# Kernel optimization log

Measured on AMD Instinct MI355X. Metric: run time of the kernel, lower is better.

## Reference

```python
import jax, jax.numpy as jnp
import numpy as np

N = 6144
IN_FEATS = 512
OUT_FEATS = 64
NHEADS = 8
ALPHA = 0.2
NEG_BIG = -9e15


def setup_inputs() -> dict:
    key = jax.random.key(0)
    k_x, k_adj, k_w, k_a1, k_a2 = jax.random.split(key, 5)
    x = jax.random.normal(k_x, (N, IN_FEATS), dtype=jnp.float32)
    adj = jax.random.randint(k_adj, (N, N), 0, 2, dtype=jnp.int32)
    # xavier_uniform with gain=1.414 ~ sqrt(2)
    gain = 1.414
    bw = gain * np.sqrt(6.0 / (IN_FEATS + OUT_FEATS))
    W = jax.random.uniform(k_w, (NHEADS, IN_FEATS, OUT_FEATS), jnp.float32, -bw, bw)
    ba = gain * np.sqrt(6.0 / (OUT_FEATS + 1))
    a1 = jax.random.uniform(k_a1, (NHEADS, OUT_FEATS), jnp.float32, -ba, ba)
    a2 = jax.random.uniform(k_a2, (NHEADS, OUT_FEATS), jnp.float32, -ba, ba)
    return {"x": x, "adj": adj, "W": W, "a1": a1, "a2": a2}


def reference(x, adj, W, a1, a2):
    # h: [H, N, F] per-head projected features
    h = jnp.einsum("ni,hif->hnf", x, W)
    s1 = jnp.einsum("hnf,hf->hn", h, a1)  # [H, N]
    s2 = jnp.einsum("hnf,hf->hn", h, a2)  # [H, N]
    # outer-sum score [H, N, N], leaky-relu, adjacency mask, row softmax
    scores = jax.nn.leaky_relu(s1[:, :, None] + s2[:, None, :], negative_slope=ALPHA)
    scores = jnp.where(adj[None] > 0, scores, NEG_BIG)
    att = jax.nn.softmax(scores, axis=-1)
    out = jnp.einsum("hnm,hmf->hnf", att, h)  # [H, N, F]
    # concat heads: [N, H*F]
    out = jnp.transpose(out, (1, 0, 2)).reshape(N, NHEADS * OUT_FEATS)
    return jax.nn.elu(out)
```

## Files before the change

kernel.cpp:

```cpp
#include <hip/hip_runtime.h>
#include <hip/hip_bf16.h>
#include <stdint.h>

#define N_NODES 6144
#define IN_F    512
#define OUT_F   64
#define NH      8
#define ALPHA   0.2f
#define L2E     1.4426950408889634f
#define NTILES  (N_NODES / 64)

typedef __attribute__((ext_vector_type(8))) short bf16x8;
typedef __attribute__((ext_vector_type(8))) _Float16 f16x8;
typedef __attribute__((ext_vector_type(4))) float f32x4;

#define MFMA16B(a, b, c) __builtin_amdgcn_mfma_f32_16x16x32_bf16(a, b, c, 0, 0, 0)
#define MFMA16H(a, b, c) __builtin_amdgcn_mfma_f32_16x16x32_f16(a, b, c, 0, 0, 0)

__device__ __forceinline__ unsigned short f2bf(float f) {
    uint32_t u = __float_as_uint(f);
    u += 0x7fffu + ((u >> 16) & 1u);
    return (unsigned short)(u >> 16);
}
__device__ __forceinline__ float bf2f(unsigned short h) {
    return __uint_as_float(((uint32_t)h) << 16);
}
__device__ __forceinline__ unsigned short f16b(float f) {
    union { _Float16 h; unsigned short u; } c;
    c.h = (_Float16)f;
    return c.u;
}
__device__ __forceinline__ uint32_t encf(float x) {
    int i = __float_as_int(x);
    return (i >= 0) ? ((uint32_t)i | 0x80000000u) : ~(uint32_t)i;
}
__device__ __forceinline__ float decf(uint32_t u) {
    int i = (u & 0x80000000u) ? (int)(u & 0x7FFFFFFFu) : ~(int)u;
    return __int_as_float(i);
}

__global__ __launch_bounds__(256) void k_prep(
    const float* __restrict__ x, unsigned short* __restrict__ xh,
    unsigned short* __restrict__ xl,
    const float* __restrict__ W, unsigned short* __restrict__ wthF,
    unsigned short* __restrict__ wtlF, uint32_t* __restrict__ s2mu,
    const int* __restrict__ adj, unsigned long long* __restrict__ bmT)
{
    const int bid = blockIdx.x;
    if (bid < 2048) {
        const int stride = 2048 * 256;
        for (int idx = bid * 256 + threadIdx.x; idx < N_NODES * N_NODES;
             idx += stride) {
            unsigned long long b = __ballot(adj[idx] > 0);
            if ((threadIdx.x & 63) == 0) {
                int r = idx / N_NODES;
                int cb = (idx % N_NODES) >> 6;
                bmT[(size_t)cb * N_NODES + r] = b;
            }
        }
    } else if (bid < 5120) {
        int i = (bid - 2048) * 256 + threadIdx.x;
        float4 v = ((const float4*)x)[i];
        float vv[4] = {v.x, v.y, v.z, v.w};
        unsigned short h4[4], l4[4];
#pragma unroll
        for (int c = 0; c < 4; ++c) {
            unsigned short hb = f2bf(vv[c]);
            h4[c] = hb;
            l4[c] = f2bf(vv[c] - bf2f(hb));
        }
        ((ushort4*)xh)[i] = make_ushort4(h4[0], h4[1], h4[2], h4[3]);
        ((ushort4*)xl)[i] = make_ushort4(l4[0], l4[1], l4[2], l4[3]);
    } else {
        int tid = (bid - 5120) * 256 + threadIdx.x;
        if (bid == 5120 && threadIdx.x < NH) s2mu[threadIdx.x] = 0u;
        int lane = tid & 63;
        int rest = tid >> 6;
        int ct = rest & 3;
        int i = (rest >> 2) & 15;
        int h = rest >> 6;
        int f = ct * 16 + (lane & 15);
        int k0 = i * 32 + (lane >> 4) * 8;
        unsigned short oh[8], ol[8];
#pragma unroll
        for (int e = 0; e < 8; ++e) {
            float wv = W[((size_t)h * IN_F + k0 + e) * OUT_F + f];
            unsigned short hb = f2bf(wv);
            oh[e] = hb;
            ol[e] = f2bf(wv - bf2f(hb));
        }
        ushort4* dh = (ushort4*)(wthF + (size_t)tid * 8);
        dh[0] = make_ushort4(oh[0], oh[1], oh[2], oh[3]);
        dh[1] = make_ushort4(oh[4], oh[5], oh[6], oh[7]);
        ushort4* dl = (ushort4*)(wtlF + (size_t)tid * 8);
        dl[0] = make_ushort4(ol[0], ol[1], ol[2], ol[3]);
        dl[1] = make_ushort4(ol[4], ol[5], ol[6], ol[7]);
    }
}

__global__ __launch_bounds__(256) void k_proj(
    const unsigned short* __restrict__ xh, const unsigned short* __restrict__ xl,
    const unsigned short* __restrict__ wthF, const unsigned short* __restrict__ wtlF,
    const float* __restrict__ a1, const float* __restrict__ a2,
    float* __restrict__ s1, float* __restrict__ s2,
    uint32_t* __restrict__ s2mu, unsigned short* __restrict__ hTF)
{
    __shared__ unsigned short hlds[64][64];

    const int head = blockIdx.x & 7;
    const int rb = blockIdx.x >> 3;
    const int w = threadIdx.x >> 6;
    const int lane = threadIdx.x & 63;
    const int r15 = lane & 15;
    const int g = lane >> 4;
    const int rowbase = rb * 64 + w * 16;
    const int rowA = rowbase + r15;

    f32x4 acc[4] = {};
    const unsigned short* xhp = xh + (size_t)rowA * IN_F + g * 8;
    const unsigned short* xlp = xl + (size_t)rowA * IN_F + g * 8;
    const unsigned short* wb = wthF + ((size_t)head * 16 * 4 * 64) * 8 + lane * 8;
    const unsigned short* wl = wtlF + ((size_t)head * 16 * 4 * 64) * 8 + lane * 8;

#pragma unroll 4
    for (int i = 0; i < 16; ++i) {
        const int k0 = i * 32;
        bf16x8 ah = *(const bf16x8*)(xhp + k0);
        bf16x8 al = *(const bf16x8*)(xlp + k0);
#pragma unroll
        for (int ct = 0; ct < 4; ++ct) {
            const size_t fo = (size_t)(i * 4 + ct) * 512;
            bf16x8 bh = *(const bf16x8*)(wb + fo);
            bf16x8 bl = *(const bf16x8*)(wl + fo);
            acc[ct] = MFMA16B(ah, bh, acc[ct]);
            acc[ct] = MFMA16B(ah, bl, acc[ct]);
            acc[ct] = MFMA16B(al, bh, acc[ct]);
        }
    }

    float a1v[4], a2v[4];
#pragma unroll
    for (int ct = 0; ct < 4; ++ct) {
        a1v[ct] = a1[head * 64 + ct * 16 + r15];
        a2v[ct] = a2[head * 64 + ct * 16 + r15];
    }
    float sp1[4] = {0, 0, 0, 0}, sp2[4] = {0, 0, 0, 0};
#pragma unroll
    for (int ct = 0; ct < 4; ++ct)
#pragma unroll
        for (int j = 0; j < 4; ++j) {
            sp1[j] += acc[ct][j] * a1v[ct];
            sp2[j] += acc[ct][j] * a2v[ct];
        }
#pragma unroll
    for (int d = 1; d < 16; d <<= 1) {
#pragma unroll
        for (int j = 0; j < 4; ++j) {
            sp1[j] += __shfl_xor(sp1[j], d);
            sp2[j] += __shfl_xor(sp2[j], d);
        }
    }
    if (r15 == 0) {
#pragma unroll
        for (int j = 0; j < 4; ++j) {
            int n = rowbase + g * 4 + j;
            s1[head * N_NODES + n] = sp1[j];
            s2[head * N_NODES + n] = sp2[j];
        }
    }
    {
        float m = fmaxf(fmaxf(sp2[0], sp2[1]), fmaxf(sp2[2], sp2[3]));
        m = fmaxf(m, __shfl_xor(m, 16));
        m = fmaxf(m, __shfl_xor(m, 32));
        if (lane == 0) atomicMax(s2mu + head, encf(m));
    }

#pragma unroll
    for (int ct = 0; ct < 4; ++ct) {
        ushort4 pk;
        pk.x = f16b(acc[ct][0]);
        pk.y = f16b(acc[ct][1]);
        pk.z = f16b(acc[ct][2]);
        pk.w = f16b(acc[ct][3]);
        int f_l = ct * 16 + r15;
        int n0 = w * 16 + g * 4;
        int col = (((n0 >> 3) ^ (f_l & 7)) << 3) + (n0 & 7);
        *(ushort4*)&hlds[f_l][col] = pk;
    }
    __syncthreads();

#pragma unroll
    for (int q = 0; q < 2; ++q) {
        int fid = 2 * w + q;
        int wk = fid >> 2, ct = fid & 3;
        int f_l = ct * 16 + (lane & 15);
        int nch = wk * 4 + (lane >> 4);
        int col = ((nch ^ (f_l & 7)) << 3);
        int4 v = *(const int4*)&hlds[f_l][col];
        size_t base = (((size_t)(head * 96 + rb)) * 8 + fid) * 512 + lane * 8;
        *(int4*)(hTF + base) = v;
    }
}

__device__ __forceinline__ f16x8 mk_pa16(int4 ep, int4 en, uint32_t e1p2,
                                         uint32_t e1n2, uint32_t ms)
{
    const uint32_t epw[4] = {(uint32_t)ep.x, (uint32_t)ep.y, (uint32_t)ep.z,
                             (uint32_t)ep.w};
    const uint32_t enw[4] = {(uint32_t)en.x, (uint32_t)en.y, (uint32_t)en.z,
                             (uint32_t)en.w};
    union { uint32_t u[4]; f16x8 v; } r;
#define PAIR(J, B0, B1)                                                       \
    {                                                                         \
        uint32_t pa, pb, pm;                                                  \
        asm("v_pk_mul_f16 %0, %1, %2" : "=v"(pa) : "v"(e1p2), "v"(epw[J]));   \
        asm("v_pk_mul_f16 %0, %1, %2" : "=v"(pb) : "v"(e1n2), "v"(enw[J]));   \
        asm("v_pk_max_f16 %0, %1, %2" : "=v"(pm) : "v"(pa), "v"(pb));         \
        uint32_t mb0, mb1;                                                    \
        asm("v_bfe_i32 %0, %1, " #B0 ", 1" : "=v"(mb0) : "v"(ms));            \
        asm("v_bfe_i32 %0, %1, " #B1 ", 1" : "=v"(mb1) : "v"(ms));            \
        r.u[J] = pm & ((mb0 & 0x0000FFFFu) | (mb1 & 0xFFFF0000u));            \
    }
    PAIR(0, 0, 1)
    PAIR(1, 2, 3)
    PAIR(2, 4, 5)
    PAIR(3, 6, 7)
#undef PAIR
    return r.v;
}

struct Pf {
    int4 hb0, hb1, hb2, hb3;
    uint32_t m0, m1;
};

__device__ __forceinline__ f16x8 as_f16x8(int4 v) {
    union { int4 i; f16x8 h; } c;
    c.i = v;
    return c.h;
}

__global__ __launch_bounds__(256, 3) void k_flash(
    const unsigned short* __restrict__ hTF, const float* __restrict__ s1,
    const float* __restrict__ s2, const uint32_t* __restrict__ s2mu,
    const uint32_t* __restrict__ bmT32, float* __restrict__ out)
{
    __shared__ uint32_t epL[3072];
    __shared__ uint32_t enL[3072];
    __shared__ float fs[128 * 20];

    const int head = blockIdx.x & 7;
    const int rb = blockIdx.x >> 3;
    const int tid = threadIdx.x;
    const int w = tid >> 6, lane = tid & 63, r15 = lane & 15, g = lane >> 4;
    const int w01 = w & 1;
    const int wk = w >> 1;
    const int shg = g * 8;

    const float s2mh = decf(s2mu[head]);
    {
        const float4* s2h = (const float4*)(s2 + head * N_NODES);
#pragma unroll
        for (int i0 = 0; i0 < 6; ++i0) {
            int i = tid + i0 * 256;
            float4 v = s2h[i];
            uint32_t p0 = f16b(exp2f((v.x - s2mh) * L2E));
            uint32_t p1 = f16b(exp2f((v.y - s2mh) * L2E));
            uint32_t p2 = f16b(exp2f((v.z - s2mh) * L2E));
            uint32_t p3 = f16b(exp2f((v.w - s2mh) * L2E));
            uint32_t n0 = f16b(exp2f(ALPHA * (v.x - s2mh) * L2E));
            uint32_t n1 = f16b(exp2f(ALPHA * (v.y - s2mh) * L2E));
            uint32_t n2 = f16b(exp2f(ALPHA * (v.z - s2mh) * L2E));
            uint32_t n3 = f16b(exp2f(ALPHA * (v.w - s2mh) * L2E));
            epL[2 * i] = p0 | (p1 << 16);
            epL[2 * i + 1] = p2 | (p3 << 16);
            enL[2 * i] = n0 | (n1 << 16);
            enL[2 * i + 1] = n2 | (n3 << 16);
        }
    }

    const int rA = rb * 64 + w01 * 32 + r15;
    const int rB = rA + 16;
    const float s1A = s1[head * N_NODES + rA];
    const float s1B = s1[head * N_NODES + rB];
    const float t0A = s1A + s2mh, t0B = s1B + s2mh;
    const float MrA = fmaxf(t0A, ALPHA * t0A);
    const float MrB = fmaxf(t0B, ALPHA * t0B);
    uint32_t E1pA2, E1nA2, E1pB2, E1nB2;
    {
        uint32_t a = f16b(exp2f((t0A - MrA) * L2E));
        uint32_t b = f16b(exp2f((ALPHA * t0A - MrA) * L2E));
        uint32_t c = f16b(exp2f((t0B - MrB) * L2E));
        uint32_t d = f16b(exp2f((ALPHA * t0B - MrB) * L2E));
        E1pA2 = a | (a << 16);
        E1nA2 = b | (b << 16);
        E1pB2 = c | (c << 16);
        E1nB2 = d | (d << 16);
    }

    const unsigned short* __restrict__ hbp =
        hTF + ((size_t)(head * 96) * 8 + wk * 4) * 512 + lane * 8;
    const uint32_t* __restrict__ epb = epL + wk * 16 + g * 4;
    const uint32_t* __restrict__ enb = enL + wk * 16 + g * 4;
    const size_t mbA = (size_t)rA * 2 + wk;
    const size_t mbB = (size_t)rB * 2 + wk;

    f32x4 accA[4] = {}, accB[4] = {};
    f32x4 accSA = {}, accSB = {};
    const f16x8 vones = {(_Float16)1.0f, (_Float16)1.0f, (_Float16)1.0f,
                         (_Float16)1.0f, (_Float16)1.0f, (_Float16)1.0f,
                         (_Float16)1.0f, (_Float16)1.0f};

    __syncthreads();

    auto loadPf = [&](int t, Pf& P) {
        const unsigned short* hp = hbp + (size_t)t * 4096;
        P.hb0 = *(const int4*)(hp);
        P.hb1 = *(const int4*)(hp + 512);
        P.hb2 = *(const int4*)(hp + 1024);
        P.hb3 = *(const int4*)(hp + 1536);
        P.m0 = bmT32[mbA + (size_t)t * 12288];
        P.m1 = bmT32[mbB + (size_t)t * 12288];
    };
    auto compute = [&](int t, Pf& C) {
        int4 ep = *(const int4*)(epb + t * 32);
        int4 en = *(const int4*)(enb + t * 32);
        f16x8 paA = mk_pa16(ep, en, E1pA2, E1nA2, C.m0 >> shg);
        f16x8 paB = mk_pa16(ep, en, E1pB2, E1nB2, C.m1 >> shg);
        accSA = MFMA16H(paA, vones, accSA);
        accSB = MFMA16H(paB, vones, accSB);
        f16x8 h0 = as_f16x8(C.hb0), h1 = as_f16x8(C.hb1);
        f16x8 h2 = as_f16x8(C.hb2), h3 = as_f16x8(C.hb3);
        accA[0] = MFMA16H(paA, h0, accA[0]);
        accB[0] = MFMA16H(paB, h0, accB[0]);
        accA[1] = MFMA16H(paA, h1, accA[1]);
        accB[1] = MFMA16H(paB, h1, accB[1]);
        accA[2] = MFMA16H(paA, h2, accA[2]);
        accB[2] = MFMA16H(paB, h2, accB[2]);
        accA[3] = MFMA16H(paA, h3, accA[3]);
        accB[3] = MFMA16H(paB, h3, accB[3]);
    };

    Pf P0, P1, P2;
    loadPf(0, P0);
    loadPf(1, P1);
    for (int t = 0; t < NTILES; t += 3) {
        loadPf(t + 2, P2);
        compute(t, P0);
        loadPf(t + 3 < NTILES ? t + 3 : NTILES - 1, P0);
        compute(t + 1, P1);
        loadPf(t + 4 < NTILES ? t + 4 : NTILES - 1, P1);
        compute(t + 2, P2);
    }

    const int slot = w01 * 64 + lane;
    const int fcb = head * 64;
    const int nA = rb * 64 + w01 * 32 + g * 4;

    if (wk == 1) {
#pragma unroll
        for (int ct = 0; ct < 4; ++ct)
#pragma unroll
            for (int j = 0; j < 4; ++j) fs[slot * 20 + ct * 4 + j] = accA[ct][j];
#pragma unroll
        for (int j = 0; j < 4; ++j) fs[slot * 20 + 16 + j] = accSA[j];
    }
    __syncthreads();
    if (wk == 0) {
        float rinv[4];
#pragma unroll
        for (int j = 0; j < 4; ++j)
            rinv[j] = 1.0f / (accSA[j] + fs[slot * 20 + 16 + j]);
#pragma unroll
        for (int ct = 0; ct < 4; ++ct)
#pragma unroll
            for (int j = 0; j < 4; ++j) {
                float v = (accA[ct][j] + fs[slot * 20 + ct * 4 + j]) * rinv[j];
                v = (v > 0.f) ? v : (expf(v) - 1.f);
                out[(size_t)(nA + j) * 512 + fcb + ct * 16 + r15] = v;
            }
    }
    __syncthreads();
    if (wk == 1) {
#pragma unroll
        for (int ct = 0; ct < 4; ++ct)
#pragma unroll
            for (int j = 0; j < 4; ++j) fs[slot * 20 + ct * 4 + j] = accB[ct][j];
#pragma unroll
        for (int j = 0; j < 4; ++j) fs[slot * 20 + 16 + j] = accSB[j];
    }
    __syncthreads();
    if (wk == 0) {
        float rinv[4];
#pragma unroll
        for (int j = 0; j < 4; ++j)
            rinv[j] = 1.0f / (accSB[j] + fs[slot * 20 + 16 + j]);
#pragma unroll
        for (int ct = 0; ct < 4; ++ct)
#pragma unroll
            for (int j = 0; j < 4; ++j) {
                float v = (accB[ct][j] + fs[slot * 20 + ct * 4 + j]) * rinv[j];
                v = (v > 0.f) ? v : (expf(v) - 1.f);
                out[(size_t)(nA + 16 + j) * 512 + fcb + ct * 16 + r15] = v;
            }
    }
}

extern "C" void kernel_launch(void* const* d_in, const int* in_sizes, int n_in,
                              void* d_out, int out_size, void* d_ws, size_t ws_size,
                              hipStream_t stream)
{
    const float* x = (const float*)d_in[0];
    const int* adj = (const int*)d_in[1];
    const float* W = (const float*)d_in[2];
    const float* a1 = (const float*)d_in[3];
    const float* a2 = (const float*)d_in[4];
    float* out = (float*)d_out;

    char* ws = (char*)d_ws;
    size_t off = 0;
    auto take = [&](size_t bytes) {
        void* p = ws + off;
        off = (off + bytes + 255) & ~(size_t)255;
        return p;
    };
    unsigned short* xh   = (unsigned short*)take((size_t)N_NODES * IN_F * 2);
    unsigned short* xl   = (unsigned short*)take((size_t)N_NODES * IN_F * 2);
    unsigned short* wthF = (unsigned short*)take((size_t)512 * 512 * 2);
    unsigned short* wtlF = (unsigned short*)take((size_t)512 * 512 * 2);
    unsigned short* hTF  = (unsigned short*)take((size_t)NH * 64 * N_NODES * 2);
    float* s1  = (float*)take((size_t)NH * N_NODES * 4);
    float* s2  = (float*)take((size_t)NH * N_NODES * 4);
    uint32_t* s2mu = (uint32_t*)take(256);
    unsigned long long* bmT =
        (unsigned long long*)take((size_t)N_NODES * (N_NODES / 64) * 8);

    k_prep<<<dim3(5248), dim3(256), 0, stream>>>(
        x, xh, xl, W, wthF, wtlF, s2mu, adj, bmT);
    k_proj<<<dim3(NH * (N_NODES / 64)), dim3(256), 0, stream>>>(
        xh, xl, wthF, wtlF, a1, a2, s1, s2, s2mu, hTF);
    k_flash<<<dim3(NH * NTILES), dim3(256), 0, stream>>>(
        hTF, s1, s2, s2mu, (const uint32_t*)bmT, out);
}
```

Measured before the change: 168.6 us.

## Hand-schedule prefetch with inline asm loads, explicit vmcnt waits, and MFMA priority

New measurement: 165.9 us. Within noise of the previous version (-1.6%).

```diff
diff --git a/kernel.cpp b/kernel.cpp
--- a/kernel.cpp
+++ b/kernel.cpp
@@ -302,8 +302,8 @@
         hTF + ((size_t)(head * 96) * 8 + wk * 4) * 512 + lane * 8;
     const uint32_t* __restrict__ epb = epL + wk * 16 + g * 4;
     const uint32_t* __restrict__ enb = enL + wk * 16 + g * 4;
-    const size_t mbA = (size_t)rA * 2 + wk;
-    const size_t mbB = (size_t)rB * 2 + wk;
+    const uint32_t* __restrict__ bmA = bmT32 + (size_t)rA * 2 + wk;
+    const uint32_t* __restrict__ bmB = bmT32 + (size_t)rB * 2 + wk;
 
     f32x4 accA[4] = {}, accB[4] = {};
     f32x4 accSA = {}, accSB = {};
@@ -315,18 +315,25 @@
 
     auto loadPf = [&](int t, Pf& P) {
         const unsigned short* hp = hbp + (size_t)t * 4096;
-        P.hb0 = *(const int4*)(hp);
-        P.hb1 = *(const int4*)(hp + 512);
-        P.hb2 = *(const int4*)(hp + 1024);
-        P.hb3 = *(const int4*)(hp + 1536);
-        P.m0 = bmT32[mbA + (size_t)t * 12288];
-        P.m1 = bmT32[mbB + (size_t)t * 12288];
+        asm volatile("global_load_dwordx4 %0, %1, off"
+                     : "=v"(P.hb0) : "v"(hp));
+        asm volatile("global_load_dwordx4 %0, %1, off offset:1024"
+                     : "=v"(P.hb1) : "v"(hp));
+        asm volatile("global_load_dwordx4 %0, %1, off offset:2048"
+                     : "=v"(P.hb2) : "v"(hp));
+        asm volatile("global_load_dwordx4 %0, %1, off offset:3072"
+                     : "=v"(P.hb3) : "v"(hp));
+        const uint32_t* pa = bmA + (size_t)t * 12288;
+        const uint32_t* pb = bmB + (size_t)t * 12288;
+        asm volatile("global_load_dword %0, %1, off" : "=v"(P.m0) : "v"(pa));
+        asm volatile("global_load_dword %0, %1, off" : "=v"(P.m1) : "v"(pb));
     };
     auto compute = [&](int t, Pf& C) {
         int4 ep = *(const int4*)(epb + t * 32);
         int4 en = *(const int4*)(enb + t * 32);
         f16x8 paA = mk_pa16(ep, en, E1pA2, E1nA2, C.m0 >> shg);
         f16x8 paB = mk_pa16(ep, en, E1pB2, E1nB2, C.m1 >> shg);
+        __builtin_amdgcn_s_setprio(1);
         accSA = MFMA16H(paA, vones, accSA);
         accSB = MFMA16H(paB, vones, accSB);
         f16x8 h0 = as_f16x8(C.hb0), h1 = as_f16x8(C.hb1);
@@ -339,19 +346,31 @@
         accB[2] = MFMA16H(paB, h2, accB[2]);
         accA[3] = MFMA16H(paA, h3, accA[3]);
         accB[3] = MFMA16H(paB, h3, accB[3]);
+        __builtin_amdgcn_s_setprio(0);
     };
 
     Pf P0, P1, P2;
     loadPf(0, P0);
     loadPf(1, P1);
+    loadPf(2, P2);
     for (int t = 0; t < NTILES; t += 3) {
-        loadPf(t + 2, P2);
+        asm volatile("s_waitcnt vmcnt(12)");
+        __builtin_amdgcn_sched_barrier(0);
         compute(t, P0);
         loadPf(t + 3 < NTILES ? t + 3 : NTILES - 1, P0);
+
+        asm volatile("s_waitcnt vmcnt(12)");
+        __builtin_amdgcn_sched_barrier(0);
         compute(t + 1, P1);
         loadPf(t + 4 < NTILES ? t + 4 : NTILES - 1, P1);
+
+        asm volatile("s_waitcnt vmcnt(12)");
+        __builtin_amdgcn_sched_barrier(0);
         compute(t + 2, P2);
-    }
+        loadPf(t + 5 < NTILES ? t + 5 : NTILES - 1, P2);
+    }
+    asm volatile("s_waitcnt vmcnt(0)");
+    __builtin_amdgcn_sched_barrier(0);
 
     const int slot = w01 * 64 + lane;
     const int fcb = head * 64;
```
